# Performance work log

Hardware: AMD Instinct MI355X
Metric: run time of the kernel (lower is better)

Reference implementation:

```python
import jax, jax.numpy as jnp
import numpy as np

WIN = 11      # pytorch_msssim default win_size
SIGMA = 1.5   # pytorch_msssim default win_sigma
K1, K2 = 0.01, 0.03
DATA_RANGE = 1.0


def _gauss_win():
    coords = np.arange(WIN, dtype=np.float64) - WIN // 2
    g = np.exp(-(coords ** 2) / (2.0 * SIGMA ** 2))
    g = g / g.sum()
    return jnp.asarray(g, dtype=jnp.float32)


def _gauss_filter(x, w):
    # x: [B, C, H, W]; separable depthwise gaussian, VALID padding (pytorch_msssim style)
    C = x.shape[1]
    dn = ('NCHW', 'OIHW', 'NCHW')
    kh = jnp.broadcast_to(w.reshape(1, 1, WIN, 1), (C, 1, WIN, 1))
    kw = jnp.broadcast_to(w.reshape(1, 1, 1, WIN), (C, 1, 1, WIN))
    x = jax.lax.conv_general_dilated(x, kh, (1, 1), 'VALID',
                                     dimension_numbers=dn, feature_group_count=C)
    x = jax.lax.conv_general_dilated(x, kw, (1, 1), 'VALID',
                                     dimension_numbers=dn, feature_group_count=C)
    return x


def _ssim_mean(X, Y):
    C1 = (K1 * DATA_RANGE) ** 2
    C2 = (K2 * DATA_RANGE) ** 2
    w = _gauss_win()
    mu1 = _gauss_filter(X, w)
    mu2 = _gauss_filter(Y, w)
    mu1_sq = mu1 * mu1
    mu2_sq = mu2 * mu2
    mu1_mu2 = mu1 * mu2
    sigma1_sq = _gauss_filter(X * X, w) - mu1_sq
    sigma2_sq = _gauss_filter(Y * Y, w) - mu2_sq
    sigma12 = _gauss_filter(X * Y, w) - mu1_mu2
    cs_map = (2.0 * sigma12 + C2) / (sigma1_sq + sigma2_sq + C2)
    ssim_map = ((2.0 * mu1_mu2 + C1) / (mu1_sq + mu2_sq + C1)) * cs_map
    return jnp.mean(ssim_map)


def setup_inputs() -> dict:
    key = jax.random.key(0)
    k1, k2 = jax.random.split(key)
    inp = jax.random.uniform(k1, (64, 1, 512, 512), dtype=jnp.float32)
    tgt = jax.random.uniform(k2, (64, 1, 512, 512), dtype=jnp.float32)
    return {"input": inp, "target": tgt}


def reference(input, target):
    # SSIMLoss.forward: 1 - SSIM(data_range=1, size_average=True, channel=1)(input, target)
    return 1.0 - _ssim_mean(input, target)
```

## Files before the change

### kernel.cpp

```cpp
#include <hip/hip_runtime.h>
#include <math.h>

#define WIN 11
#define OH 32
#define OW 64
#define IW 74
#define VSTR 84
#define PLANE (OH * VSTR)
#define IMG 512
#define OUTD 502
#define NIMG 64

struct GW { float w[WIN]; };

__global__ __launch_bounds__(64) void ssim_zero(double* acc) {
    acc[0] = 0.0;
}

__global__ __launch_bounds__(256) void ssim_kernel(
    const float* __restrict__ X, const float* __restrict__ Y,
    double* __restrict__ acc, GW gw)
{
    __shared__ float vb[5 * PLANE];
    __shared__ float red[4];

    const int tid = threadIdx.x;
    const int tC = blockIdx.x, tR = blockIdx.y, b = blockIdx.z;
    const int gr0 = tR * OH, gc0 = tC * OW;
    const float* __restrict__ Xb = X + (size_t)b * (IMG * IMG);
    const float* __restrict__ Yb = Y + (size_t)b * (IMG * IMG);

    if (tid < 152) {
        const int rg = tid / 19, cg = tid - rg * 19;
        const int r0 = rg * 4;
        int gc = gc0 + cg * 4;
        if (gc > IMG - 4) gc = IMG - 4;

        float a[5][4][4] = {};
        #pragma unroll
        for (int k = 0; k < 4 + WIN - 1; ++k) {
            int gr = gr0 + r0 + k; if (gr > IMG - 1) gr = IMG - 1;
            const float4 xv = *reinterpret_cast<const float4*>(Xb + (size_t)gr * IMG + gc);
            const float4 yv = *reinterpret_cast<const float4*>(Yb + (size_t)gr * IMG + gc);
            float xs[4] = {xv.x, xv.y, xv.z, xv.w};
            float ys[4] = {yv.x, yv.y, yv.z, yv.w};
            float xx[4], yy[4], xy[4];
            #pragma unroll
            for (int c = 0; c < 4; ++c) {
                xx[c] = xs[c] * xs[c];
                yy[c] = ys[c] * ys[c];
                xy[c] = xs[c] * ys[c];
            }
            #pragma unroll
            for (int i2 = 0; i2 < 4; ++i2) {
                const int t = k - i2;
                if (t >= 0 && t < WIN) {
                    const float wt = gw.w[t];
                    #pragma unroll
                    for (int c = 0; c < 4; ++c) {
                        a[0][i2][c] += wt * xs[c];
                        a[1][i2][c] += wt * ys[c];
                        a[2][i2][c] += wt * xx[c];
                        a[3][i2][c] += wt * yy[c];
                        a[4][i2][c] += wt * xy[c];
                    }
                }
            }
        }
        #pragma unroll
        for (int ch = 0; ch < 5; ++ch) {
            #pragma unroll
            for (int i2 = 0; i2 < 4; ++i2) {
                float4 v = make_float4(a[ch][i2][0], a[ch][i2][1],
                                       a[ch][i2][2], a[ch][i2][3]);
                *reinterpret_cast<float4*>(&vb[ch * PLANE + (r0 + i2) * VSTR + cg * 4]) = v;
            }
        }
    }
    __syncthreads();

    const int r  = tid >> 3;
    const int c0 = (tid & 7) * 8;
    const float* vrow = &vb[r * VSTR + c0];

    float m[5][8];
    #pragma unroll
    for (int ch = 0; ch < 5; ++ch) {
        const float* p = vrow + ch * PLANE;
        float w18[18];
        *reinterpret_cast<float4*>(&w18[0])  = *reinterpret_cast<const float4*>(p);
        *reinterpret_cast<float4*>(&w18[4])  = *reinterpret_cast<const float4*>(p + 4);
        *reinterpret_cast<float4*>(&w18[8])  = *reinterpret_cast<const float4*>(p + 8);
        *reinterpret_cast<float4*>(&w18[12]) = *reinterpret_cast<const float4*>(p + 12);
        *reinterpret_cast<float2*>(&w18[16]) = *reinterpret_cast<const float2*>(p + 16);
        #pragma unroll
        for (int o = 0; o < 8; ++o) {
            float s = 0.f;
            #pragma unroll
            for (int t = 0; t < WIN; ++t) s += gw.w[t] * w18[o + t];
            m[ch][o] = s;
        }
    }

    const float C1 = 1e-4f, C2 = 9e-4f;
    float lsum = 0.f;
    const int ogr = gr0 + r;
    #pragma unroll
    for (int o = 0; o < 8; ++o) {
        const int ogc = gc0 + c0 + o;
        float mu1 = m[0][o], mu2 = m[1][o];
        float mu1s = mu1 * mu1, mu2s = mu2 * mu2, m12 = mu1 * mu2;
        float s1  = m[2][o] - mu1s;
        float s2  = m[3][o] - mu2s;
        float s12 = m[4][o] - m12;
        float num = (2.f * s12 + C2) * (2.f * m12 + C1);
        float den = (s1 + s2 + C2) * (mu1s + mu2s + C1);
        float ss  = num * __builtin_amdgcn_rcpf(den);
        if (ogr < OUTD && ogc < OUTD) lsum += ss;
    }

    #pragma unroll
    for (int off = 32; off > 0; off >>= 1)
        lsum += __shfl_down(lsum, off, 64);
    if ((tid & 63) == 0) red[tid >> 6] = lsum;
    __syncthreads();
    if (tid == 0) {
        float bs = red[0] + red[1] + red[2] + red[3];
        atomicAdd(acc, (double)bs);
    }
}

__global__ void ssim_finalize(const double* __restrict__ acc,
                              float* __restrict__ out) {
    out[0] = 1.0f - (float)(acc[0] / (double)((long long)NIMG * OUTD * OUTD));
}

extern "C" void kernel_launch(void* const* d_in, const int* in_sizes, int n_in,
                              void* d_out, int out_size, void* d_ws, size_t ws_size,
                              hipStream_t stream) {
    const float* X = (const float*)d_in[0];
    const float* Y = (const float*)d_in[1];
    double* acc = (double*)d_ws;
    float* out = (float*)d_out;

    GW gw;
    double c[WIN], s = 0.0;
    for (int i = 0; i < WIN; ++i) {
        double d = (double)i - (double)(WIN / 2);
        c[i] = exp(-(d * d) / (2.0 * 1.5 * 1.5));
        s += c[i];
    }
    for (int i = 0; i < WIN; ++i) gw.w[i] = (float)(c[i] / s);

    ssim_zero<<<1, 64, 0, stream>>>(acc);
    dim3 grid(IMG / OW, IMG / OH, NIMG);
    ssim_kernel<<<grid, 256, 0, stream>>>(X, Y, acc, gw);
    ssim_finalize<<<1, 1, 0, stream>>>(acc, out);
}
```

Baseline: 121.7 us.

## Halve tile height, use packed f32x2 math, and raise occupancy

Shrinks the output tile from 32 to 16 rows, so each vertical-pass thread covers 2 rows instead of 4 and each horizontal-pass thread produces 4 outputs instead of 8. The vertical accumulation now uses 2-wide float vectors so the compiler can emit packed FMA instructions. It also adds a min-blocks hint of 5 and narrows the LDS row stride to cut shared memory and register use. In exchange, the vertical halo is re-read more often (12 input rows per 2 outputs instead of 14 per 4), which raises global load traffic and doubles the block count.

Measured after the change: 224.6 us. +84.5%, slower.

```diff
diff --git a/kernel.cpp b/kernel.cpp
--- a/kernel.cpp
+++ b/kernel.cpp
@@ -2,14 +2,15 @@
 #include <math.h>
 
 #define WIN 11
-#define OH 32
+#define OH 16
 #define OW 64
-#define IW 74
-#define VSTR 84
+#define VSTR 76
 #define PLANE (OH * VSTR)
 #define IMG 512
 #define OUTD 502
 #define NIMG 64
+
+typedef float f32x2 __attribute__((ext_vector_type(2)));
 
 struct GW { float w[WIN]; };
 
@@ -17,7 +18,7 @@
     acc[0] = 0.0;
 }
 
-__global__ __launch_bounds__(256) void ssim_kernel(
+__global__ __launch_bounds__(256, 5) void ssim_kernel(
     const float* __restrict__ X, const float* __restrict__ Y,
     double* __restrict__ acc, GW gw)
 {
@@ -32,72 +33,64 @@
 
     if (tid < 152) {
         const int rg = tid / 19, cg = tid - rg * 19;
-        const int r0 = rg * 4;
+        const int r0 = rg * 2;
         int gc = gc0 + cg * 4;
         if (gc > IMG - 4) gc = IMG - 4;
 
-        float a[5][4][4] = {};
+        f32x2 a[5][2][2] = {};
         #pragma unroll
-        for (int k = 0; k < 4 + WIN - 1; ++k) {
+        for (int k = 0; k < 2 + WIN - 1; ++k) {
             int gr = gr0 + r0 + k; if (gr > IMG - 1) gr = IMG - 1;
             const float4 xv = *reinterpret_cast<const float4*>(Xb + (size_t)gr * IMG + gc);
             const float4 yv = *reinterpret_cast<const float4*>(Yb + (size_t)gr * IMG + gc);
-            float xs[4] = {xv.x, xv.y, xv.z, xv.w};
-            float ys[4] = {yv.x, yv.y, yv.z, yv.w};
-            float xx[4], yy[4], xy[4];
+            f32x2 x0 = {xv.x, xv.y}, x1 = {xv.z, xv.w};
+            f32x2 y0 = {yv.x, yv.y}, y1 = {yv.z, yv.w};
+            f32x2 xx0 = x0 * x0, xx1 = x1 * x1;
+            f32x2 yy0 = y0 * y0, yy1 = y1 * y1;
+            f32x2 xy0 = x0 * y0, xy1 = x1 * y1;
             #pragma unroll
-            for (int c = 0; c < 4; ++c) {
-                xx[c] = xs[c] * xs[c];
-                yy[c] = ys[c] * ys[c];
-                xy[c] = xs[c] * ys[c];
-            }
-            #pragma unroll
-            for (int i2 = 0; i2 < 4; ++i2) {
+            for (int i2 = 0; i2 < 2; ++i2) {
                 const int t = k - i2;
                 if (t >= 0 && t < WIN) {
                     const float wt = gw.w[t];
-                    #pragma unroll
-                    for (int c = 0; c < 4; ++c) {
-                        a[0][i2][c] += wt * xs[c];
-                        a[1][i2][c] += wt * ys[c];
-                        a[2][i2][c] += wt * xx[c];
-                        a[3][i2][c] += wt * yy[c];
-                        a[4][i2][c] += wt * xy[c];
-                    }
+                    a[0][i2][0] += wt * x0;  a[0][i2][1] += wt * x1;
+                    a[1][i2][0] += wt * y0;  a[1][i2][1] += wt * y1;
+                    a[2][i2][0] += wt * xx0; a[2][i2][1] += wt * xx1;
+                    a[3][i2][0] += wt * yy0; a[3][i2][1] += wt * yy1;
+                    a[4][i2][0] += wt * xy0; a[4][i2][1] += wt * xy1;
                 }
             }
         }
         #pragma unroll
         for (int ch = 0; ch < 5; ++ch) {
             #pragma unroll
-            for (int i2 = 0; i2 < 4; ++i2) {
-                float4 v = make_float4(a[ch][i2][0], a[ch][i2][1],
-                                       a[ch][i2][2], a[ch][i2][3]);
+            for (int i2 = 0; i2 < 2; ++i2) {
+                float4 v = make_float4(a[ch][i2][0].x, a[ch][i2][0].y,
+                                       a[ch][i2][1].x, a[ch][i2][1].y);
                 *reinterpret_cast<float4*>(&vb[ch * PLANE + (r0 + i2) * VSTR + cg * 4]) = v;
             }
         }
     }
     __syncthreads();
 
-    const int r  = tid >> 3;
-    const int c0 = (tid & 7) * 8;
+    const int r  = tid >> 4;
+    const int c0 = (tid & 15) * 4;
     const float* vrow = &vb[r * VSTR + c0];
 
-    float m[5][8];
+    float m[5][4];
     #pragma unroll
     for (int ch = 0; ch < 5; ++ch) {
         const float* p = vrow + ch * PLANE;
-        float w18[18];
-        *reinterpret_cast<float4*>(&w18[0])  = *reinterpret_cast<const float4*>(p);
-        *reinterpret_cast<float4*>(&w18[4])  = *reinterpret_cast<const float4*>(p + 4);
-        *reinterpret_cast<float4*>(&w18[8])  = *reinterpret_cast<const float4*>(p + 8);
-        *reinterpret_cast<float4*>(&w18[12]) = *reinterpret_cast<const float4*>(p + 12);
-        *reinterpret_cast<float2*>(&w18[16]) = *reinterpret_cast<const float2*>(p + 16);
+        float w14[14];
+        *reinterpret_cast<float4*>(&w14[0])  = *reinterpret_cast<const float4*>(p);
+        *reinterpret_cast<float4*>(&w14[4])  = *reinterpret_cast<const float4*>(p + 4);
+        *reinterpret_cast<float4*>(&w14[8])  = *reinterpret_cast<const float4*>(p + 8);
+        *reinterpret_cast<float2*>(&w14[12]) = *reinterpret_cast<const float2*>(p + 12);
         #pragma unroll
-        for (int o = 0; o < 8; ++o) {
+        for (int o = 0; o < 4; ++o) {
             float s = 0.f;
             #pragma unroll
-            for (int t = 0; t < WIN; ++t) s += gw.w[t] * w18[o + t];
+            for (int t = 0; t < WIN; ++t) s += gw.w[t] * w14[o + t];
             m[ch][o] = s;
         }
     }
@@ -106,7 +99,7 @@
     float lsum = 0.f;
     const int ogr = gr0 + r;
     #pragma unroll
-    for (int o = 0; o < 8; ++o) {
+    for (int o = 0; o < 4; ++o) {
         const int ogc = gc0 + c0 + o;
         float mu1 = m[0][o], mu2 = m[1][o];
         float mu1s = mu1 * mu1, mu2s = mu2 * mu2, m12 = mu1 * mu2;
```

## Store vertical-pass sums in fp16 LDS and do horizontal pass with packed half math

Applied to the files above, without the earlier changes.

Vertical Gaussian pass now has all 256 threads each handle 2 columns using packed float2 math. The five intermediate planes are stored in LDS as fp16, which halves shared memory and allows more resident blocks. The horizontal pass runs as packed fp16 FMAs with even/odd shifted pairs. Tiles are retiled to 54 output columns with a 10-wide grid so that halo overlap covers the image without clamped waste. The fp16 accumulation of the sigma terms (E[x^2] minus mu^2) risks cancellation error and may hurt accuracy.

After: 146.2 us. +20.2%, slower.

```diff
diff --git a/kernel.cpp b/kernel.cpp
--- a/kernel.cpp
+++ b/kernel.cpp
@@ -3,25 +3,37 @@
 
 #define WIN 11
 #define OH 32
-#define OW 64
-#define IW 74
-#define VSTR 84
-#define PLANE (OH * VSTR)
+#define OW 54
+#define IWV 64
+#define VSTRH 64
+#define PLANEH (OH * VSTRH)
 #define IMG 512
 #define OUTD 502
 #define NIMG 64
+#define NTX 10
 
-struct GW { float w[WIN]; };
+typedef float    f32x2 __attribute__((ext_vector_type(2)));
+typedef _Float16 h2    __attribute__((ext_vector_type(2)));
+typedef _Float16 h8    __attribute__((ext_vector_type(8)));
+
+struct GW {
+    float    wf[WIN];
+    unsigned whp[WIN];
+};
+
+__device__ inline h2 wsplat(unsigned u) {
+    union { unsigned u; h2 h; } x; x.u = u; return x.h;
+}
 
 __global__ __launch_bounds__(64) void ssim_zero(double* acc) {
-    acc[0] = 0.0;
+    if (threadIdx.x == 0) acc[0] = 0.0;
 }
 
-__global__ __launch_bounds__(256) void ssim_kernel(
+__global__ __launch_bounds__(256, 4) void ssim_kernel(
     const float* __restrict__ X, const float* __restrict__ Y,
     double* __restrict__ acc, GW gw)
 {
-    __shared__ float vb[5 * PLANE];
+    __shared__ _Float16 vb[5 * PLANEH];
     __shared__ float red[4];
 
     const int tid = threadIdx.x;
@@ -30,40 +42,31 @@
     const float* __restrict__ Xb = X + (size_t)b * (IMG * IMG);
     const float* __restrict__ Yb = Y + (size_t)b * (IMG * IMG);
 
-    if (tid < 152) {
-        const int rg = tid / 19, cg = tid - rg * 19;
+    {
+        const int rg = tid >> 5, cg = tid & 31;
         const int r0 = rg * 4;
-        int gc = gc0 + cg * 4;
-        if (gc > IMG - 4) gc = IMG - 4;
+        int gc = gc0 + cg * 2;
+        if (gc > IMG - 2) gc = IMG - 2;
 
-        float a[5][4][4] = {};
+        f32x2 a[5][4] = {};
         #pragma unroll
         for (int k = 0; k < 4 + WIN - 1; ++k) {
             int gr = gr0 + r0 + k; if (gr > IMG - 1) gr = IMG - 1;
-            const float4 xv = *reinterpret_cast<const float4*>(Xb + (size_t)gr * IMG + gc);
-            const float4 yv = *reinterpret_cast<const float4*>(Yb + (size_t)gr * IMG + gc);
-            float xs[4] = {xv.x, xv.y, xv.z, xv.w};
-            float ys[4] = {yv.x, yv.y, yv.z, yv.w};
-            float xx[4], yy[4], xy[4];
-            #pragma unroll
-            for (int c = 0; c < 4; ++c) {
-                xx[c] = xs[c] * xs[c];
-                yy[c] = ys[c] * ys[c];
-                xy[c] = xs[c] * ys[c];
-            }
+            const float2 xv = *reinterpret_cast<const float2*>(Xb + (size_t)gr * IMG + gc);
+            const float2 yv = *reinterpret_cast<const float2*>(Yb + (size_t)gr * IMG + gc);
+            f32x2 x = {xv.x, xv.y};
+            f32x2 y = {yv.x, yv.y};
+            f32x2 xx = x * x, yy = y * y, xy = x * y;
             #pragma unroll
             for (int i2 = 0; i2 < 4; ++i2) {
                 const int t = k - i2;
                 if (t >= 0 && t < WIN) {
-                    const float wt = gw.w[t];
-                    #pragma unroll
-                    for (int c = 0; c < 4; ++c) {
-                        a[0][i2][c] += wt * xs[c];
-                        a[1][i2][c] += wt * ys[c];
-                        a[2][i2][c] += wt * xx[c];
-                        a[3][i2][c] += wt * yy[c];
-                        a[4][i2][c] += wt * xy[c];
-                    }
+                    const float wt = gw.wf[t];
+                    a[0][i2] += wt * x;
+                    a[1][i2] += wt * y;
+                    a[2][i2] += wt * xx;
+                    a[3][i2] += wt * yy;
+                    a[4][i2] += wt * xy;
                 }
             }
         }
@@ -71,52 +74,71 @@
         for (int ch = 0; ch < 5; ++ch) {
             #pragma unroll
             for (int i2 = 0; i2 < 4; ++i2) {
-                float4 v = make_float4(a[ch][i2][0], a[ch][i2][1],
-                                       a[ch][i2][2], a[ch][i2][3]);
-                *reinterpret_cast<float4*>(&vb[ch * PLANE + (r0 + i2) * VSTR + cg * 4]) = v;
+                h2 hv = { (_Float16)a[ch][i2].x, (_Float16)a[ch][i2].y };
+                *reinterpret_cast<h2*>(&vb[ch * PLANEH + (r0 + i2) * VSTRH + cg * 2]) = hv;
             }
         }
     }
     __syncthreads();
 
-    const int r  = tid >> 3;
-    const int c0 = (tid & 7) * 8;
-    const float* vrow = &vb[r * VSTR + c0];
+    const int r   = tid >> 3;
+    const int c0h = (tid & 7) * 8;
+    const _Float16* rb = &vb[r * VSTRH];
 
-    float m[5][8];
+    const int b1 = (c0h == 56) ? 56 : c0h + 8;
+    int b2 = c0h + 16; if (b2 > 62) b2 = 62;
+
+    h2 m[5][4];
     #pragma unroll
     for (int ch = 0; ch < 5; ++ch) {
-        const float* p = vrow + ch * PLANE;
-        float w18[18];
-        *reinterpret_cast<float4*>(&w18[0])  = *reinterpret_cast<const float4*>(p);
-        *reinterpret_cast<float4*>(&w18[4])  = *reinterpret_cast<const float4*>(p + 4);
-        *reinterpret_cast<float4*>(&w18[8])  = *reinterpret_cast<const float4*>(p + 8);
-        *reinterpret_cast<float4*>(&w18[12]) = *reinterpret_cast<const float4*>(p + 12);
-        *reinterpret_cast<float2*>(&w18[16]) = *reinterpret_cast<const float2*>(p + 16);
+        const _Float16* p = rb + ch * PLANEH;
+        h8 v0 = *reinterpret_cast<const h8*>(p + c0h);
+        h8 v1 = *reinterpret_cast<const h8*>(p + b1);
+        h2 e8 = *reinterpret_cast<const h2*>(p + b2);
+        h2 e[9];
         #pragma unroll
-        for (int o = 0; o < 8; ++o) {
-            float s = 0.f;
+        for (int j = 0; j < 4; ++j) { e[j] = h2{ v0[2*j], v0[2*j+1] }; }
+        #pragma unroll
+        for (int j = 0; j < 4; ++j) { e[4+j] = h2{ v1[2*j], v1[2*j+1] }; }
+        e[8] = e8;
+        h2 o[8];
+        #pragma unroll
+        for (int j = 0; j < 8; ++j) { o[j] = h2{ e[j][1], e[j+1][0] }; }
+
+        #pragma unroll
+        for (int pr = 0; pr < 4; ++pr) {
+            h2 s = h2{ (_Float16)0, (_Float16)0 };
             #pragma unroll
-            for (int t = 0; t < WIN; ++t) s += gw.w[t] * w18[o + t];
-            m[ch][o] = s;
+            for (int u = 0; u < 6; ++u)
+                s += wsplat(gw.whp[2*u]) * e[pr + u];
+            #pragma unroll
+            for (int u = 0; u < 5; ++u)
+                s += wsplat(gw.whp[2*u+1]) * o[pr + u];
+            m[ch][pr] = s;
         }
     }
 
     const float C1 = 1e-4f, C2 = 9e-4f;
+    int cmax = OUTD - gc0; if (cmax > OW) cmax = OW;
+    const int rmax = OUTD - gr0;
+    const bool rowok = (r < rmax);
+
     float lsum = 0.f;
-    const int ogr = gr0 + r;
     #pragma unroll
-    for (int o = 0; o < 8; ++o) {
-        const int ogc = gc0 + c0 + o;
-        float mu1 = m[0][o], mu2 = m[1][o];
-        float mu1s = mu1 * mu1, mu2s = mu2 * mu2, m12 = mu1 * mu2;
-        float s1  = m[2][o] - mu1s;
-        float s2  = m[3][o] - mu2s;
-        float s12 = m[4][o] - m12;
-        float num = (2.f * s12 + C2) * (2.f * m12 + C1);
-        float den = (s1 + s2 + C2) * (mu1s + mu2s + C1);
-        float ss  = num * __builtin_amdgcn_rcpf(den);
-        if (ogr < OUTD && ogc < OUTD) lsum += ss;
+    for (int pr = 0; pr < 4; ++pr) {
+        #pragma unroll
+        for (int h = 0; h < 2; ++h) {
+            float mu1 = (float)m[0][pr][h];
+            float mu2 = (float)m[1][pr][h];
+            float mu1s = mu1 * mu1, mu2s = mu2 * mu2, m12 = mu1 * mu2;
+            float s1  = (float)m[2][pr][h] - mu1s;
+            float s2  = (float)m[3][pr][h] - mu2s;
+            float s12 = (float)m[4][pr][h] - m12;
+            float num = (2.f * s12 + C2) * (2.f * m12 + C1);
+            float den = (s1 + s2 + C2) * (mu1s + mu2s + C1);
+            float ss  = num * __builtin_amdgcn_rcpf(den);
+            if (rowok && (c0h + 2*pr + h) < cmax) lsum += ss;
+        }
     }
 
     #pragma unroll
@@ -135,6 +157,18 @@
     out[0] = 1.0f - (float)(acc[0] / (double)((long long)NIMG * OUTD * OUTD));
 }
 
+static unsigned short f2h_rne(float f) {
+    union { float f; unsigned u; } v; v.f = f;
+    unsigned u = v.u;
+    unsigned s = (u >> 16) & 0x8000u;
+    int e = (int)((u >> 23) & 0xff) - 112;
+    unsigned mant = u & 0x7fffffu;
+    unsigned h = s | ((unsigned)e << 10) | (mant >> 13);
+    unsigned rem = mant & 0x1fffu;
+    if (rem > 0x1000u || (rem == 0x1000u && (h & 1u))) h++;
+    return (unsigned short)h;
+}
+
 extern "C" void kernel_launch(void* const* d_in, const int* in_sizes, int n_in,
                               void* d_out, int out_size, void* d_ws, size_t ws_size,
                               hipStream_t stream) {
@@ -150,10 +184,15 @@
         c[i] = exp(-(d * d) / (2.0 * 1.5 * 1.5));
         s += c[i];
     }
-    for (int i = 0; i < WIN; ++i) gw.w[i] = (float)(c[i] / s);
+    for (int i = 0; i < WIN; ++i) {
+        float w = (float)(c[i] / s);
+        gw.wf[i] = w;
+        unsigned short hb = f2h_rne(w);
+        gw.whp[i] = (unsigned)hb | ((unsigned)hb << 16);
+    }
 
     ssim_zero<<<1, 64, 0, stream>>>(acc);
-    dim3 grid(IMG / OW, IMG / OH, NIMG);
+    dim3 grid(NTX, IMG / OH, NIMG);
     ssim_kernel<<<grid, 256, 0, stream>>>(X, Y, acc, gw);
     ssim_finalize<<<1, 1, 0, stream>>>(acc, out);
 }
```
